# Optimization experiments

Measured on AMD Instinct MI355X. Metric: run time of the kernel, lower is better.

## Reference

```python
import jax, jax.numpy as jnp
import numpy as np

D_MODEL = 1024

def setup_inputs() -> dict:
    key = jax.random.key(0)
    ks = jax.random.split(key, 7)
    B, S, D = 4, 2048, D_MODEL
    scale = 1.0 / np.sqrt(D)
    x = jax.random.normal(ks[0], (B, S, D), dtype=jnp.float32)
    Wq = jax.random.normal(ks[1], (D, D), dtype=jnp.float32) * scale
    bq = jnp.zeros((D,), dtype=jnp.float32)
    Wk = jax.random.normal(ks[2], (D, D), dtype=jnp.float32) * scale
    bk = jnp.zeros((D,), dtype=jnp.float32)
    Wv = jax.random.normal(ks[3], (D, D), dtype=jnp.float32) * scale
    bv = jnp.zeros((D,), dtype=jnp.float32)
    return {"x": x, "Wq": Wq, "bq": bq, "Wk": Wk, "bk": bk, "Wv": Wv, "bv": bv}

def reference(x, Wq, bq, Wk, bk, Wv, bv):
    # Single-head attention; scale = 1/sqrt(d_model) as in the torch module (self.d_k = d_model).
    d_k = x.shape[-1]
    q = jnp.einsum('bsd,de->bse', x, Wq) + bq
    k = jnp.einsum('bsd,de->bse', x, Wk) + bk
    v = jnp.einsum('bsd,de->bse', x, Wv) + bv
    scores = jnp.einsum('bqd,bkd->bqk', q, k) / jnp.sqrt(jnp.asarray(d_k, x.dtype))
    attn = jax.nn.softmax(scores, axis=-1)
    return jnp.einsum('bqk,bkd->bqd', attn, v)
```

## Files before the change

### kernel.cpp

```cpp
#include <hip/hip_runtime.h>
#include <hip/hip_bf16.h>

#define DM 1024
#define SEQ 2048
#define NBATCH 4

using f32x4 = __attribute__((ext_vector_type(4))) float;
using s16x8 = __attribute__((ext_vector_type(8))) short;
using u16x4 = __attribute__((ext_vector_type(4))) unsigned short;
using u16x8 = __attribute__((ext_vector_type(8))) unsigned short;

__device__ __forceinline__ unsigned short f2bf(float f) {
  union { float f; unsigned u; } v; v.f = f;
  return (unsigned short)((v.u + 0x7fffu + ((v.u >> 16) & 1u)) >> 16);
}

__device__ __forceinline__ void g2lds16(const void* g, void* l) {
  __builtin_amdgcn_global_load_lds(
      (const __attribute__((address_space(1))) void*)g,
      (__attribute__((address_space(3))) void*)l, 16, 0, 0);
}


__global__ void cvt_x(const float* __restrict__ X, unsigned short* __restrict__ XB) {
  const int i = blockIdx.x * 256 + threadIdx.x;
  const f32x4* p = (const f32x4*)X;
  f32x4 a = p[2 * i], b = p[2 * i + 1];
  u16x8 o;
#pragma unroll
  for (int q = 0; q < 4; q++) { o[q] = f2bf(a[q]); o[4 + q] = f2bf(b[q]); }
  *(u16x8*)(XB + (size_t)i * 8) = o;
}

__global__ void transpose_w(const float* __restrict__ Wq, const float* __restrict__ Wk,
                            const float* __restrict__ Wv, unsigned short* __restrict__ WT) {
  const int seg = blockIdx.z;
  const float* W = (seg == 0) ? Wq : (seg == 1) ? Wk : Wv;
  unsigned short* out = WT + (size_t)seg * DM * DM;
  __shared__ float t[32][33];
  const int k0 = blockIdx.y * 32, n0 = blockIdx.x * 32;
  const int tr = threadIdx.x >> 5, tc = threadIdx.x & 31;
#pragma unroll
  for (int p = 0; p < 4; p++) {
    int r = tr + p * 8;
    t[r][tc] = W[(size_t)(k0 + r) * DM + n0 + tc];
  }
  __syncthreads();
#pragma unroll
  for (int p = 0; p < 4; p++) {
    int r = tr + p * 8;
    out[(size_t)(n0 + r) * DM + k0 + tc] = f2bf(t[tc][r]);
  }
}

template <int MODE, int LDA, int LDB, int KDIM>
__global__ void gemm_nt(const unsigned short* __restrict__ A,
                        const unsigned short* __restrict__ B,
                        void* __restrict__ C0,
                        unsigned short* __restrict__ C1,
                        unsigned short* __restrict__ C2,
                        const float* __restrict__ bq,
                        const float* __restrict__ bk,
                        const float* __restrict__ bv) {
  __shared__ unsigned short lA[128 * 32];
  __shared__ unsigned short lB[128 * 32];

  const int tid = threadIdx.x;
  const int w = tid >> 6;
  const int L = tid & 63;
  const int wm = w & 1, wn = w >> 1;
  const int bz = blockIdx.z;
  const int tileM = blockIdx.y * 128, tileN = blockIdx.x * 128;

  const unsigned short* Ab = A;
  const unsigned short* Bb = B;
  if (MODE == 1) { Ab += (size_t)bz * SEQ * DM; Bb += (size_t)bz * SEQ * DM; }
  if (MODE == 2) { Ab += (size_t)bz * SEQ * SEQ; Bb += (size_t)bz * DM * SEQ; }

  const int rowA0 = tid >> 2;
  const char* gA0 = (const char*)(Ab + (size_t)(tileM + rowA0) * LDA) + (tid & 3) * 16;
  const char* gB0 = (const char*)(Bb + (size_t)(tileN + rowA0) * LDB) + (tid & 3) * 16;
  const size_t strA64 = (size_t)64 * LDA * 2;
  const size_t strB64 = (size_t)64 * LDB * 2;
  char* lAbase = (char*)lA + w * 1024;
  char* lBbase = (char*)lB + w * 1024;

  f32x4 acc[4][4];
#pragma unroll
  for (int i = 0; i < 4; i++)
#pragma unroll
    for (int j = 0; j < 4; j++) acc[i][j] = (f32x4){0.f, 0.f, 0.f, 0.f};

  for (int k = 0; k < KDIM; k += 32) {
    const size_t kb = (size_t)k * 2;
    g2lds16(gA0 + kb,          lAbase);
    g2lds16(gA0 + strA64 + kb, lAbase + 4096);
    g2lds16(gB0 + kb,          lBbase);
    g2lds16(gB0 + strB64 + kb, lBbase + 4096);
    __syncthreads();

    s16x8 av[4], bv4[4];
#pragma unroll
    for (int i = 0; i < 4; i++)
      av[i] = *(const s16x8*)&lA[(wm * 64 + i * 16 + (L & 15)) * 32 + (L >> 4) * 8];
#pragma unroll
    for (int j = 0; j < 4; j++)
      bv4[j] = *(const s16x8*)&lB[(wn * 64 + j * 16 + (L & 15)) * 32 + (L >> 4) * 8];
#pragma unroll
    for (int i = 0; i < 4; i++)
#pragma unroll
      for (int j = 0; j < 4; j++)
        acc[i][j] = __builtin_amdgcn_mfma_f32_16x16x32_bf16(av[i], bv4[j], acc[i][j], 0, 0, 0);
    __syncthreads();
  }

#pragma unroll
  for (int i = 0; i < 4; i++) {
    const int gm0 = tileM + wm * 64 + i * 16 + (L >> 4) * 4;
#pragma unroll
    for (int j = 0; j < 4; j++) {
      const int gn = tileN + wn * 64 + j * 16 + (L & 15);
      if (MODE == 0) {
        const int seg = gn >> 10;
        const int colin = gn & 1023;
        if (seg == 0) {
          const float bias = bq[colin];
          unsigned short* Q = (unsigned short*)C0;
#pragma unroll
          for (int r = 0; r < 4; r++) Q[(size_t)(gm0 + r) * DM + colin] = f2bf(acc[i][j][r] + bias);
        } else if (seg == 1) {
          const float bias = bk[colin];
#pragma unroll
          for (int r = 0; r < 4; r++) C1[(size_t)(gm0 + r) * DM + colin] = f2bf(acc[i][j][r] + bias);
        } else {
          const float bias = bv[colin];
          u16x4 pk;
#pragma unroll
          for (int r = 0; r < 4; r++) pk[r] = f2bf(acc[i][j][r] + bias);
          const int b = gm0 >> 11, s0 = gm0 & 2047;
          *(u16x4*)(C2 + ((size_t)((b << 10) + colin)) * SEQ + s0) = pk;
        }
      } else if (MODE == 1) {
        float* S = (float*)C0 + (size_t)bz * SEQ * SEQ;
#pragma unroll
        for (int r = 0; r < 4; r++) S[(size_t)(gm0 + r) * SEQ + gn] = acc[i][j][r] * 0.03125f;
      } else {
        float* O = (float*)C0 + (size_t)bz * SEQ * DM;
#pragma unroll
        for (int r = 0; r < 4; r++) O[(size_t)(gm0 + r) * DM + gn] = acc[i][j][r];
      }
    }
  }
}

__global__ void softmax_k(const float* __restrict__ S, unsigned short* __restrict__ P) {
  const int row = blockIdx.x;
  const float* src = S + (size_t)row * SEQ;
  const int t = threadIdx.x;
  f32x4 a = *(const f32x4*)(src + t * 8);
  f32x4 b = *(const f32x4*)(src + t * 8 + 4);
  float m = fmaxf(fmaxf(fmaxf(a[0], a[1]), fmaxf(a[2], a[3])),
                  fmaxf(fmaxf(b[0], b[1]), fmaxf(b[2], b[3])));
#pragma unroll
  for (int o = 32; o > 0; o >>= 1) m = fmaxf(m, __shfl_down(m, o, 64));
  __shared__ float redm[4], reds[4];
  if ((t & 63) == 0) redm[t >> 6] = m;
  __syncthreads();
  m = fmaxf(fmaxf(redm[0], redm[1]), fmaxf(redm[2], redm[3]));
  float e[8]; float s = 0.f;
#pragma unroll
  for (int q = 0; q < 4; q++) { e[q] = __expf(a[q] - m); s += e[q]; }
#pragma unroll
  for (int q = 0; q < 4; q++) { e[4 + q] = __expf(b[q] - m); s += e[4 + q]; }
#pragma unroll
  for (int o = 32; o > 0; o >>= 1) s += __shfl_down(s, o, 64);
  if ((t & 63) == 0) reds[t >> 6] = s;
  __syncthreads();
  s = reds[0] + reds[1] + reds[2] + reds[3];
  const float inv = 1.0f / s;
  u16x8 o8;
#pragma unroll
  for (int q = 0; q < 8; q++) o8[q] = f2bf(e[q] * inv);
  *(u16x8*)(P + (size_t)row * SEQ + t * 8) = o8;
}

extern "C" void kernel_launch(void* const* d_in, const int* in_sizes, int n_in,
                              void* d_out, int out_size, void* d_ws, size_t ws_size,
                              hipStream_t stream) {
  (void)in_sizes; (void)n_in; (void)out_size; (void)ws_size;
  const float* x  = (const float*)d_in[0];
  const float* Wq = (const float*)d_in[1];
  const float* bq = (const float*)d_in[2];
  const float* Wk = (const float*)d_in[3];
  const float* bk = (const float*)d_in[4];
  const float* Wv = (const float*)d_in[5];
  const float* bv = (const float*)d_in[6];
  float* out = (float*)d_out;
  char* ws = (char*)d_ws;
  unsigned short* xb = (unsigned short*)(ws + 0);
  unsigned short* wt = (unsigned short*)(ws + 16777216);
  unsigned short* qb = (unsigned short*)(ws + 23068672);
  unsigned short* kb = (unsigned short*)(ws + 39845888);
  unsigned short* vt = (unsigned short*)(ws + 56623104);
  float*          S  = (float*)         (ws + 73400320);
  unsigned short* P  = (unsigned short*)(ws + 140509184);

  cvt_x<<<4096, 256, 0, stream>>>(x, xb);
  transpose_w<<<dim3(32, 32, 3), 256, 0, stream>>>(Wq, Wk, Wv, wt);
  gemm_nt<0, 1024, 1024, 1024><<<dim3(24, 64, 1), 256, 0, stream>>>(
      xb, wt, (void*)qb, kb, vt, bq, bk, bv);
  gemm_nt<1, 1024, 1024, 1024><<<dim3(16, 16, 4), 256, 0, stream>>>(
      qb, kb, (void*)S, nullptr, nullptr, nullptr, nullptr, nullptr);
  softmax_k<<<8192, 256, 0, stream>>>(S, P);
  gemm_nt<2, 2048, 2048, 2048><<<dim3(8, 16, 4), 256, 0, stream>>>(
      P, vt, (void*)out, nullptr, nullptr, nullptr, nullptr, nullptr);
}
```

Measured before the change: 294.9 us.

## Double-buffer LDS tiles in GEMM and XOR-swizzle chunks against bank conflicts

```diff
diff --git a/kernel.cpp b/kernel.cpp
--- a/kernel.cpp
+++ b/kernel.cpp
@@ -62,8 +62,8 @@
                         const float* __restrict__ bq,
                         const float* __restrict__ bk,
                         const float* __restrict__ bv) {
-  __shared__ unsigned short lA[128 * 32];
-  __shared__ unsigned short lB[128 * 32];
+  __shared__ unsigned short lA[2][128 * 32];
+  __shared__ unsigned short lB[2][128 * 32];
 
   const int tid = threadIdx.x;
   const int w = tid >> 6;
@@ -77,13 +77,24 @@
   if (MODE == 1) { Ab += (size_t)bz * SEQ * DM; Bb += (size_t)bz * SEQ * DM; }
   if (MODE == 2) { Ab += (size_t)bz * SEQ * SEQ; Bb += (size_t)bz * DM * SEQ; }
 
-  const int rowA0 = tid >> 2;
-  const char* gA0 = (const char*)(Ab + (size_t)(tileM + rowA0) * LDA) + (tid & 3) * 16;
-  const char* gB0 = (const char*)(Bb + (size_t)(tileN + rowA0) * LDB) + (tid & 3) * 16;
+  const int srow = tid >> 2;
+  const int gch = (tid & 3) ^ (srow & 3);
+  const char* gA0 = (const char*)(Ab + (size_t)(tileM + srow) * LDA) + gch * 16;
+  const char* gB0 = (const char*)(Bb + (size_t)(tileN + srow) * LDB) + gch * 16;
   const size_t strA64 = (size_t)64 * LDA * 2;
   const size_t strB64 = (size_t)64 * LDB * 2;
-  char* lAbase = (char*)lA + w * 1024;
-  char* lBbase = (char*)lB + w * 1024;
+  char* lAw = (char*)lA + w * 1024;
+  char* lBw = (char*)lB + w * 1024;
+
+#define STAGE(kt, b) do {                                          \
+    const size_t kb_ = (size_t)(kt) * 64;                          \
+    char* la_ = lAw + (b) * 8192;                                  \
+    char* lb_ = lBw + (b) * 8192;                                  \
+    g2lds16(gA0 + kb_,          la_);                              \
+    g2lds16(gA0 + strA64 + kb_, la_ + 4096);                       \
+    g2lds16(gB0 + kb_,          lb_);                              \
+    g2lds16(gB0 + strB64 + kb_, lb_ + 4096);                       \
+  } while (0)
 
   f32x4 acc[4][4];
 #pragma unroll
@@ -91,28 +102,31 @@
 #pragma unroll
     for (int j = 0; j < 4; j++) acc[i][j] = (f32x4){0.f, 0.f, 0.f, 0.f};
 
-  for (int k = 0; k < KDIM; k += 32) {
-    const size_t kb = (size_t)k * 2;
-    g2lds16(gA0 + kb,          lAbase);
-    g2lds16(gA0 + strA64 + kb, lAbase + 4096);
-    g2lds16(gB0 + kb,          lBbase);
-    g2lds16(gB0 + strB64 + kb, lBbase + 4096);
+  const int rl = L & 15;
+  const int pc = ((L >> 4) ^ (rl & 3)) * 8;
+
+  constexpr int NK = KDIM / 32;
+  STAGE(0, 0);
+
+  for (int k = 0; k < NK; ++k) {
     __syncthreads();
-
+    if (k + 1 < NK) STAGE(k + 1, (k + 1) & 1);
+    const unsigned short* cA = lA[k & 1];
+    const unsigned short* cB = lB[k & 1];
     s16x8 av[4], bv4[4];
 #pragma unroll
     for (int i = 0; i < 4; i++)
-      av[i] = *(const s16x8*)&lA[(wm * 64 + i * 16 + (L & 15)) * 32 + (L >> 4) * 8];
+      av[i] = *(const s16x8*)&cA[(wm * 64 + i * 16 + rl) * 32 + pc];
 #pragma unroll
     for (int j = 0; j < 4; j++)
-      bv4[j] = *(const s16x8*)&lB[(wn * 64 + j * 16 + (L & 15)) * 32 + (L >> 4) * 8];
+      bv4[j] = *(const s16x8*)&cB[(wn * 64 + j * 16 + rl) * 32 + pc];
 #pragma unroll
     for (int i = 0; i < 4; i++)
 #pragma unroll
       for (int j = 0; j < 4; j++)
         acc[i][j] = __builtin_amdgcn_mfma_f32_16x16x32_bf16(av[i], bv4[j], acc[i][j], 0, 0, 0);
-    __syncthreads();
-  }
+  }
+#undef STAGE
 
 #pragma unroll
   for (int i = 0; i < 4; i++) {
```

Result: no change. 298.5 us (+1.2%).
